# Kernel tuning notes

Measured on AMD Instinct MI355X. Metric: run time of the kernel, lower is better.

## Reference

```python
import jax, jax.numpy as jnp
import numpy as np

NEG_BIG = -9e15
ALPHA = 0.2  # LeakyReLU negative slope


def setup_inputs() -> dict:
    key = jax.random.key(0)
    k1, k2, k3, k4 = jax.random.split(key, 4)
    N, F_in, F_out = 8192, 256, 64
    inp = jax.random.normal(k1, (N, F_in), dtype=jnp.float32)
    adj = jax.random.randint(k2, (N, N), 0, 2, dtype=jnp.int32)
    W = jax.random.normal(k3, (F_in, F_out), dtype=jnp.float32) * 0.05
    a = jax.random.normal(k4, (2 * F_out, 1), dtype=jnp.float32) * 0.05
    return {"input": inp, "adj": adj, "W": W, "a": a}


def reference(input, adj, W, a):
    # h = X W : [N, F_out]
    h = input @ W
    F_out = W.shape[1]
    # a_input[i,j] = concat(h_i, h_j); a_input @ a = h@a1 broadcast over j + h@a2 broadcast over i.
    a1 = a[:F_out, 0]   # [F_out]
    a2 = a[F_out:, 0]   # [F_out]
    s1 = h @ a1         # [N]
    s2 = h @ a2         # [N]
    e = jax.nn.leaky_relu(s1[:, None] + s2[None, :], negative_slope=ALPHA)  # [N, N]
    att = jnp.where(adj > 0, e, jnp.float32(NEG_BIG))
    att = jax.nn.softmax(att, axis=1)
    # dropout is identity in eval mode (training=False)
    h_prime = att @ h   # [N, F_out]
    return jax.nn.elu(h_prime)
```

## Files before the change

### kernel.cpp

```cpp
#include <hip/hip_runtime.h>
#include <hip/hip_bf16.h>

typedef __bf16 bf16_t;
typedef __attribute__((ext_vector_type(8))) __bf16 bf16x8;
typedef __attribute__((ext_vector_type(4))) __bf16 bf16x4;
typedef __attribute__((ext_vector_type(4))) float floatx4;
typedef __attribute__((ext_vector_type(4))) int intx4;

#define NN 8192
#define FIN 256
#define FOUT 64
#define GAT_ALPHA 0.2f
#define NSLICE 8
#define JS (NN / NSLICE)

__global__ __launch_bounds__(256) void gat_h_kernel(
    const float* __restrict__ input,
    const float* __restrict__ W,
    const float* __restrict__ a,
    bf16_t* __restrict__ hT,
    float* __restrict__ s1g, float* __restrict__ e1g, float* __restrict__ f1g,
    float* __restrict__ s2g, float* __restrict__ e2g, float* __restrict__ f2g)
{
    alignas(16) __shared__ bf16_t in_lds[32][264];
    alignas(16) __shared__ bf16_t wt_lds[64][264];
    __shared__ float h_lds[32][65];

    const int t  = threadIdx.x;
    const int i0 = blockIdx.x * 32;

    #pragma unroll
    for (int v = 0; v < 8; v++) {
        int u  = v * 256 + t;
        int i  = u >> 6;
        int k4 = (u & 63) * 4;
        floatx4 x = *(const floatx4*)(input + (size_t)(i0 + i) * FIN + k4);
        bf16x4 b;
        #pragma unroll
        for (int e = 0; e < 4; e++) b[e] = (bf16_t)x[e];
        *(bf16x4*)(&in_lds[i][k4]) = b;
    }
    #pragma unroll
    for (int v = 0; v < 16; v++) {
        int u  = v * 256 + t;
        int k  = u >> 4;
        int f4 = (u & 15) * 4;
        floatx4 wv = *(const floatx4*)(W + k * FOUT + f4);
        #pragma unroll
        for (int e = 0; e < 4; e++) wt_lds[f4 + e][k] = (bf16_t)wv[e];
    }
    __syncthreads();

    const int wave = t >> 6;
    const int lane = t & 63;
    const int i16  = (wave & 1) * 16;
    const int f32  = (wave >> 1) * 32;
    const int lm   = lane & 15;
    const int lq   = lane >> 4;

    floatx4 acc0 = {0.f, 0.f, 0.f, 0.f};
    floatx4 acc1 = {0.f, 0.f, 0.f, 0.f};
    #pragma unroll
    for (int ks = 0; ks < 8; ks++) {
        int ko = ks * 32 + lq * 8;
        bf16x8 af = *(const bf16x8*)(&in_lds[i16 + lm][ko]);
        bf16x8 b0 = *(const bf16x8*)(&wt_lds[f32 + lm][ko]);
        bf16x8 b1 = *(const bf16x8*)(&wt_lds[f32 + 16 + lm][ko]);
        acc0 = __builtin_amdgcn_mfma_f32_16x16x32_bf16(af, b0, acc0, 0, 0, 0);
        acc1 = __builtin_amdgcn_mfma_f32_16x16x32_bf16(af, b1, acc1, 0, 0, 0);
    }

    #pragma unroll
    for (int c = 0; c < 2; c++) {
        floatx4 acc = c ? acc1 : acc0;
        int f  = f32 + c * 16 + lm;
        int ib = i0 + i16 + lq * 4;
        bf16x4 hp;
        #pragma unroll
        for (int r = 0; r < 4; r++) hp[r] = (bf16_t)acc[r];
        *(bf16x4*)(hT + (size_t)f * NN + ib) = hp;
    }
    #pragma unroll
    for (int c = 0; c < 2; c++) {
        floatx4 acc = c ? acc1 : acc0;
        #pragma unroll
        for (int r = 0; r < 4; r++)
            h_lds[i16 + lq * 4 + r][f32 + c * 16 + lm] = acc[r];
    }
    __syncthreads();

    if (t < 64) {
        int r   = t & 31;
        int sel = t >> 5;
        const float* av = a + sel * FOUT;
        float s = 0.f;
        #pragma unroll 8
        for (int f = 0; f < FOUT; f++) s += h_lds[r][f] * av[f];
        int gi = i0 + r;
        float E = expf(s);
        float F = expf(GAT_ALPHA * s);
        if (sel == 0) { s1g[gi] = s; e1g[gi] = E; f1g[gi] = F; }
        else          { s2g[gi] = s; e2g[gi] = E; f2g[gi] = F; }
    }
}

#define LOADB(B, J)                                                           \
    {                                                                         \
        B##a0 = *(const intx4*)(adjp + (J));                                  \
        B##a1 = *(const intx4*)(adjp + (J) + 4);                              \
        B##h0 = *(const bf16x8*)(hp + (size_t)0  * NN + (J));                 \
        B##h1 = *(const bf16x8*)(hp + (size_t)16 * NN + (J));                 \
        B##h2 = *(const bf16x8*)(hp + (size_t)32 * NN + (J));                 \
        B##h3 = *(const bf16x8*)(hp + (size_t)48 * NN + (J));                 \
    }

#define COMP(B, JL)                                                           \
    {                                                                         \
        int oo = (JL) + lq * 8;                                               \
        floatx4 e2a = *(const floatx4*)(&e2l[oo]);                            \
        floatx4 e2b = *(const floatx4*)(&e2l[oo + 4]);                        \
        floatx4 f2a = *(const floatx4*)(&f2l[oo]);                            \
        floatx4 f2b = *(const floatx4*)(&f2l[oo + 4]);                        \
        bf16x8 frag;                                                          \
        _Pragma("unroll")                                                     \
        for (int e = 0; e < 4; e++) {                                         \
            float w0 = fmaxf(E1 * e2a[e], F1 * f2a[e]);                       \
            w0 = (B##a0[e] > 0) ? w0 : 0.f;                                   \
            frag[e] = (bf16_t)w0;                                             \
            float w1 = fmaxf(E1 * e2b[e], F1 * f2b[e]);                       \
            w1 = (B##a1[e] > 0) ? w1 : 0.f;                                   \
            frag[e + 4] = (bf16_t)w1;                                         \
        }                                                                     \
        acc0 = __builtin_amdgcn_mfma_f32_16x16x32_bf16(frag, B##h0, acc0,0,0,0); \
        acc1 = __builtin_amdgcn_mfma_f32_16x16x32_bf16(frag, B##h1, acc1,0,0,0); \
        acc2 = __builtin_amdgcn_mfma_f32_16x16x32_bf16(frag, B##h2, acc2,0,0,0); \
        acc3 = __builtin_amdgcn_mfma_f32_16x16x32_bf16(frag, B##h3, acc3,0,0,0); \
        accR = __builtin_amdgcn_mfma_f32_16x16x32_bf16(frag, ones, accR,0,0,0);  \
    }

__global__ __launch_bounds__(256, 4) void gat_att_kernel(
    const int* __restrict__ adj,
    const bf16_t* __restrict__ hT,
    const float* __restrict__ e1g, const float* __restrict__ f1g,
    const float* __restrict__ e2g, const float* __restrict__ f2g,
    float* __restrict__ pacc,
    float* __restrict__ prs)
{
    __shared__ float e2l[JS];
    __shared__ float f2l[JS];

    const int t     = threadIdx.x;
    const int i0    = blockIdx.x * 64;
    const int slice = blockIdx.y;
    const int jbase = slice * JS;

    {
        int o = t * 4;
        *(floatx4*)(&e2l[o]) = *(const floatx4*)(e2g + jbase + o);
        *(floatx4*)(&f2l[o]) = *(const floatx4*)(f2g + jbase + o);
    }
    __syncthreads();

    const int wave = t >> 6;
    const int lane = t & 63;
    const int lm   = lane & 15;
    const int lq   = lane >> 4;
    const int row  = i0 + wave * 16 + lm;

    const float E1 = e1g[row];
    const float F1 = f1g[row];

    const int*    adjp = adj + (size_t)row * NN + jbase + lq * 8;
    const bf16_t* hp   = hT + (size_t)lm * NN + jbase + lq * 8;

    floatx4 acc0 = {0.f,0.f,0.f,0.f}, acc1 = {0.f,0.f,0.f,0.f};
    floatx4 acc2 = {0.f,0.f,0.f,0.f}, acc3 = {0.f,0.f,0.f,0.f};
    floatx4 accR = {0.f,0.f,0.f,0.f};

    bf16x8 ones;
    #pragma unroll
    for (int e = 0; e < 8; e++) ones[e] = (bf16_t)1.0f;

    intx4 Xa0, Xa1; bf16x8 Xh0, Xh1, Xh2, Xh3;
    intx4 Ya0, Ya1; bf16x8 Yh0, Yh1, Yh2, Yh3;

    LOADB(X, 0);
    for (int jl = 0; jl < JS; jl += 64) {
        int jn1 = jl + 32;
        LOADB(Y, jn1);
        COMP(X, jl);
        int jn2 = (jl + 64 < JS) ? (jl + 64) : 0;
        LOADB(X, jn2);
        COMP(Y, jn1);
    }

    if (lm == 0) {
        #pragma unroll
        for (int r = 0; r < 4; r++)
            prs[(size_t)slice * NN + i0 + wave * 16 + lq * 4 + r] = accR[r];
    }

    float* pa = pacc + (size_t)slice * NN * FOUT + (size_t)(i0 + wave * 16) * FOUT;
    #pragma unroll
    for (int c = 0; c < 4; c++) {
        floatx4 acc = (c == 0) ? acc0 : (c == 1) ? acc1 : (c == 2) ? acc2 : acc3;
        #pragma unroll
        for (int r = 0; r < 4; r++)
            pa[(size_t)(lq * 4 + r) * FOUT + c * 16 + lm] = acc[r];
    }
}

__global__ __launch_bounds__(256) void gat_combine_kernel(
    const float* __restrict__ pacc,
    const float* __restrict__ prs,
    float* __restrict__ out)
{
    int idx = blockIdx.x * 256 + threadIdx.x;
    int i   = idx >> 4;
    floatx4 s = {0.f, 0.f, 0.f, 0.f};
    float rs  = 0.f;
    #pragma unroll
    for (int p = 0; p < NSLICE; p++) {
        floatx4 v = *(const floatx4*)(pacc + (size_t)p * NN * FOUT + (size_t)idx * 4);
        s += v;
        rs += prs[p * NN + i];
    }
    float rinv = (rs > 0.f) ? 1.0f / rs : 0.f;
    floatx4 r;
    #pragma unroll
    for (int e = 0; e < 4; e++) {
        float x = s[e] * rinv;
        r[e] = (x > 0.f) ? x : (expf(x) - 1.0f);
    }
    *(floatx4*)(out + (size_t)idx * 4) = r;
}

extern "C" void kernel_launch(void* const* d_in, const int* in_sizes, int n_in,
                              void* d_out, int out_size, void* d_ws, size_t ws_size,
                              hipStream_t stream) {
    const float* input = (const float*)d_in[0];
    const int*   adj   = (const int*)d_in[1];
    const float* W     = (const float*)d_in[2];
    const float* a     = (const float*)d_in[3];
    float*       out   = (float*)d_out;

    char* ws = (char*)d_ws;
    bf16_t* hT  = (bf16_t*)ws;
    float*  s1g = (float*)(ws + (1 << 20));
    float*  e1g = s1g + NN;
    float*  f1g = e1g + NN;
    float*  s2g = f1g + NN;
    float*  e2g = s2g + NN;
    float*  f2g = e2g + NN;
    float*  pacc = f2g + NN;
    float*  prs  = pacc + (size_t)NSLICE * NN * FOUT;

    gat_h_kernel<<<NN / 32, 256, 0, stream>>>(input, W, a, hT,
                                              s1g, e1g, f1g, s2g, e2g, f2g);
    dim3 gridB(NN / 64, NSLICE);
    gat_att_kernel<<<gridB, 256, 0, stream>>>(adj, hT, e1g, f1g, e2g, f2g,
                                              pacc, prs);
    gat_combine_kernel<<<NN * FOUT / 4 / 256, 256, 0, stream>>>(pacc, prs, out);
}
```

Before: 438.8 us.

## Stage adj and hT tiles through LDS with async global_load_lds double buffering

Replaces direct per-lane register loads of adj and hT in the attention kernel with asynchronous global-to-LDS copies into swizzled double buffers, synchronised with vmcnt waits and barriers. Blocks now cover 32 rows, with waves split across row halves and feature halves, and NSLICE doubles to 16 to raise grid size. The goal is coalesced, latency-hidden streaming of the adjacency matrix, which dominates memory traffic. In exchange it adds barriers and LDS traffic, and the doubled slice count doubles the partial-accumulator writes and reads in the combine kernel.

```diff
diff --git a/kernel.cpp b/kernel.cpp
--- a/kernel.cpp
+++ b/kernel.cpp
@@ -11,8 +11,14 @@
 #define FIN 256
 #define FOUT 64
 #define GAT_ALPHA 0.2f
-#define NSLICE 8
+#define NSLICE 16
 #define JS (NN / NSLICE)
+#define NCH (JS / 64)
+
+typedef const __attribute__((address_space(1))) void gv_t;
+typedef __attribute__((address_space(3))) void lv_t;
+#define GLOAD16(gp, lp) \
+    __builtin_amdgcn_global_load_lds((gv_t*)(gp), (lv_t*)(lp), 16, 0, 0)
 
 __global__ __launch_bounds__(256) void gat_h_kernel(
     const float* __restrict__ input,
@@ -104,40 +110,6 @@
     }
 }
 
-#define LOADB(B, J)                                                           \
-    {                                                                         \
-        B##a0 = *(const intx4*)(adjp + (J));                                  \
-        B##a1 = *(const intx4*)(adjp + (J) + 4);                              \
-        B##h0 = *(const bf16x8*)(hp + (size_t)0  * NN + (J));                 \
-        B##h1 = *(const bf16x8*)(hp + (size_t)16 * NN + (J));                 \
-        B##h2 = *(const bf16x8*)(hp + (size_t)32 * NN + (J));                 \
-        B##h3 = *(const bf16x8*)(hp + (size_t)48 * NN + (J));                 \
-    }
-
-#define COMP(B, JL)                                                           \
-    {                                                                         \
-        int oo = (JL) + lq * 8;                                               \
-        floatx4 e2a = *(const floatx4*)(&e2l[oo]);                            \
-        floatx4 e2b = *(const floatx4*)(&e2l[oo + 4]);                        \
-        floatx4 f2a = *(const floatx4*)(&f2l[oo]);                            \
-        floatx4 f2b = *(const floatx4*)(&f2l[oo + 4]);                        \
-        bf16x8 frag;                                                          \
-        _Pragma("unroll")                                                     \
-        for (int e = 0; e < 4; e++) {                                         \
-            float w0 = fmaxf(E1 * e2a[e], F1 * f2a[e]);                       \
-            w0 = (B##a0[e] > 0) ? w0 : 0.f;                                   \
-            frag[e] = (bf16_t)w0;                                             \
-            float w1 = fmaxf(E1 * e2b[e], F1 * f2b[e]);                       \
-            w1 = (B##a1[e] > 0) ? w1 : 0.f;                                   \
-            frag[e + 4] = (bf16_t)w1;                                         \
-        }                                                                     \
-        acc0 = __builtin_amdgcn_mfma_f32_16x16x32_bf16(frag, B##h0, acc0,0,0,0); \
-        acc1 = __builtin_amdgcn_mfma_f32_16x16x32_bf16(frag, B##h1, acc1,0,0,0); \
-        acc2 = __builtin_amdgcn_mfma_f32_16x16x32_bf16(frag, B##h2, acc2,0,0,0); \
-        acc3 = __builtin_amdgcn_mfma_f32_16x16x32_bf16(frag, B##h3, acc3,0,0,0); \
-        accR = __builtin_amdgcn_mfma_f32_16x16x32_bf16(frag, ones, accR,0,0,0);  \
-    }
-
 __global__ __launch_bounds__(256, 4) void gat_att_kernel(
     const int* __restrict__ adj,
     const bf16_t* __restrict__ hT,
@@ -146,67 +118,120 @@
     float* __restrict__ pacc,
     float* __restrict__ prs)
 {
-    __shared__ float e2l[JS];
-    __shared__ float f2l[JS];
+    __shared__ int    adjL[2][32][64];
+    alignas(16) __shared__ bf16_t htL[2][64][64];
+    __shared__ float  e2l[JS], f2l[JS];
 
     const int t     = threadIdx.x;
-    const int i0    = blockIdx.x * 64;
+    const int i0    = blockIdx.x * 32;
     const int slice = blockIdx.y;
     const int jbase = slice * JS;
-
-    {
-        int o = t * 4;
-        *(floatx4*)(&e2l[o]) = *(const floatx4*)(e2g + jbase + o);
-        *(floatx4*)(&f2l[o]) = *(const floatx4*)(f2g + jbase + o);
-    }
-    __syncthreads();
 
     const int wave = t >> 6;
     const int lane = t & 63;
     const int lm   = lane & 15;
     const int lq   = lane >> 4;
-    const int row  = i0 + wave * 16 + lm;
-
-    const float E1 = e1g[row];
-    const float F1 = f1g[row];
-
-    const int*    adjp = adj + (size_t)row * NN + jbase + lq * 8;
-    const bf16_t* hp   = hT + (size_t)lm * NN + jbase + lq * 8;
+    const int wm   = wave & 1;
+    const int wf   = wave >> 1;
+    const int xm   = lm & 7;
+
+    {
+        const float* src = (wave & 2) ? f2g : e2g;
+        float*       dst = (wave & 2) ? f2l : e2l;
+        int off = (wave & 1) * 256;
+        GLOAD16(src + jbase + off + lane * 4, dst + off);
+    }
+
+    auto stage = [&](int b, int c) {
+        const int jg = jbase + c * 64;
+        #pragma unroll
+        for (int h = 0; h < 2; h++) {
+            int r0 = wave * 8 + h * 4;
+            int i  = r0 + (lane >> 4);
+            int gl = (lane & 15) ^ (i & 7);
+            GLOAD16(adj + (size_t)(i0 + i) * NN + jg + gl * 4,
+                    &adjL[b][r0][0]);
+        }
+        #pragma unroll
+        for (int h = 0; h < 2; h++) {
+            int f0 = wave * 16 + h * 8;
+            int f  = f0 + (lane >> 3);
+            int gl = (lane & 7) ^ (f & 7);
+            GLOAD16(hT + (size_t)f * NN + jg + gl * 8,
+                    &htL[b][f0][0]);
+        }
+    };
+
+    stage(0, 0);
+    stage(1, 1);
+
+    const int   row = i0 + wm * 16 + lm;
+    const float E1  = e1g[row];
+    const float F1  = f1g[row];
 
     floatx4 acc0 = {0.f,0.f,0.f,0.f}, acc1 = {0.f,0.f,0.f,0.f};
-    floatx4 acc2 = {0.f,0.f,0.f,0.f}, acc3 = {0.f,0.f,0.f,0.f};
     floatx4 accR = {0.f,0.f,0.f,0.f};
-
     bf16x8 ones;
     #pragma unroll
     for (int e = 0; e < 8; e++) ones[e] = (bf16_t)1.0f;
 
-    intx4 Xa0, Xa1; bf16x8 Xh0, Xh1, Xh2, Xh3;
-    intx4 Ya0, Ya1; bf16x8 Yh0, Yh1, Yh2, Yh3;
-
-    LOADB(X, 0);
-    for (int jl = 0; jl < JS; jl += 64) {
-        int jn1 = jl + 32;
-        LOADB(Y, jn1);
-        COMP(X, jl);
-        int jn2 = (jl + 64 < JS) ? (jl + 64) : 0;
-        LOADB(X, jn2);
-        COMP(Y, jn1);
-    }
-
-    if (lm == 0) {
+    #pragma unroll
+    for (int c = 0; c < NCH; c++) {
+        const int b = c & 1;
+        if (c + 1 < NCH) asm volatile("s_waitcnt vmcnt(4)" ::: "memory");
+        else             asm volatile("s_waitcnt vmcnt(0)" ::: "memory");
+        __builtin_amdgcn_s_barrier();
+        asm volatile("" ::: "memory");
+
+        const char* aB = (const char*)&adjL[b][wm * 16 + lm][0];
+        const char* hB = (const char*)&htL[b][0][0];
+        const int   j0 = c * 64;
+        #pragma unroll
+        for (int ks = 0; ks < 2; ks++) {
+            intx4 a0 = *(const intx4*)(aB + (((ks * 8 + lq * 2 + 0) ^ xm) << 4));
+            intx4 a1 = *(const intx4*)(aB + (((ks * 8 + lq * 2 + 1) ^ xm) << 4));
+            int jo = j0 + ks * 32 + lq * 8;
+            floatx4 e2a = *(const floatx4*)(&e2l[jo]);
+            floatx4 e2b = *(const floatx4*)(&e2l[jo + 4]);
+            floatx4 f2a = *(const floatx4*)(&f2l[jo]);
+            floatx4 f2b = *(const floatx4*)(&f2l[jo + 4]);
+            bf16x8 frag;
+            #pragma unroll
+            for (int e = 0; e < 4; e++) {
+                float w0 = fmaxf(E1 * e2a[e], F1 * f2a[e]);
+                frag[e]     = (bf16_t)((a0[e] > 0) ? w0 : 0.f);
+                float w1 = fmaxf(E1 * e2b[e], F1 * f2b[e]);
+                frag[e + 4] = (bf16_t)((a1[e] > 0) ? w1 : 0.f);
+            }
+            int gh = ((ks * 4 + lq) ^ xm) << 4;
+            bf16x8 b0 = *(const bf16x8*)(hB + (wf * 32 + lm) * 128 + gh);
+            bf16x8 b1 = *(const bf16x8*)(hB + (wf * 32 + 16 + lm) * 128 + gh);
+            acc0 = __builtin_amdgcn_mfma_f32_16x16x32_bf16(frag, b0, acc0, 0, 0, 0);
+            acc1 = __builtin_amdgcn_mfma_f32_16x16x32_bf16(frag, b1, acc1, 0, 0, 0);
+            if (wf == 0)
+                accR = __builtin_amdgcn_mfma_f32_16x16x32_bf16(frag, ones, accR, 0, 0, 0);
+        }
+
+        asm volatile("" ::: "memory");
+        __builtin_amdgcn_s_barrier();
+        asm volatile("" ::: "memory");
+        if (c + 2 < NCH) stage(b, c + 2);
+    }
+
+    if (wf == 0 && lm == 0) {
         #pragma unroll
         for (int r = 0; r < 4; r++)
-            prs[(size_t)slice * NN + i0 + wave * 16 + lq * 4 + r] = accR[r];
-    }
-
-    float* pa = pacc + (size_t)slice * NN * FOUT + (size_t)(i0 + wave * 16) * FOUT;
-    #pragma unroll
-    for (int c = 0; c < 4; c++) {
-        floatx4 acc = (c == 0) ? acc0 : (c == 1) ? acc1 : (c == 2) ? acc2 : acc3;
+            prs[(size_t)slice * NN + i0 + wm * 16 + lq * 4 + r] = accR[r];
+    }
+
+    float* pa = pacc + (size_t)slice * NN * FOUT
+                     + (size_t)(i0 + wm * 16) * FOUT;
+    #pragma unroll
+    for (int ft = 0; ft < 2; ft++) {
+        floatx4 acc = ft ? acc1 : acc0;
         #pragma unroll
         for (int r = 0; r < 4; r++)
-            pa[(size_t)(lq * 4 + r) * FOUT + c * 16 + lm] = acc[r];
+            pa[(size_t)(lq * 4 + r) * FOUT + wf * 32 + ft * 16 + lm] = acc[r];
     }
 }
 
@@ -257,7 +282,7 @@
 
     gat_h_kernel<<<NN / 32, 256, 0, stream>>>(input, W, a, hT,
                                               s1g, e1g, f1g, s2g, e2g, f2g);
-    dim3 gridB(NN / 64, NSLICE);
+    dim3 gridB(NN / 32, NSLICE);
     gat_att_kernel<<<gridB, 256, 0, stream>>>(adj, hT, e1g, f1g, e2g, f2g,
                                               pacc, prs);
     gat_combine_kernel<<<NN * FOUT / 4 / 256, 256, 0, stream>>>(pacc, prs, out);
```

New measurement: 398.5 us. 1.1x faster.
